# Kernel optimization log

Measured on AMD Instinct MI355X. Metric: run time of the kernel, lower is better.

## Reference

```python
import jax, jax.numpy as jnp
import numpy as np

B, IN_NUM, IN_DIM = 64, 4096, 8
NUM_CAPS, DIM_CAPS, ROUTINGS = 32, 16, 3
EPS = 1e-7  # keras.backend.epsilon()


def squash(v, axis=-1):
    # squash(s) = ||s||^2/(1+||s||^2) * s/||s||
    s2 = jnp.sum(v * v, axis=axis, keepdims=True)
    return (s2 / (1.0 + s2)) * v / jnp.sqrt(s2 + EPS)


def setup_inputs() -> dict:
    key = jax.random.key(0)
    k1, k2 = jax.random.split(key)
    inputs = jax.random.normal(k1, (B, IN_NUM, IN_DIM), dtype=jnp.float32)
    # kernel: [num_capsule, input_num_capsule, dim_capsule, input_dim_capsule]
    W = jax.random.normal(k2, (NUM_CAPS, IN_NUM, DIM_CAPS, IN_DIM), dtype=jnp.float32) * 0.05
    return {"inputs": inputs, "W": W}


def reference(inputs, W):
    # prediction vectors u_hat[b,c,n,j] = sum_i W[c,n,j,i] * x[b,n,i]
    hat = jnp.einsum('bni,cnji->bcnj', inputs, W)  # [B, C, N, D]
    b = jnp.zeros(hat.shape[:3], hat.dtype)        # routing logits [B, C, N]
    out = None
    for i in range(ROUTINGS):
        c = jax.nn.softmax(b, axis=1)              # couple over output capsules
        out = squash(jnp.einsum('bcn,bcnj->bcj', c, hat))  # [B, C, D]
        if i < ROUTINGS - 1:
            b = b + jnp.einsum('bcj,bcnj->bcn', out, hat)  # agreement update
    return out
```

## Files before the change

### kernel.cpp

```cpp
#include <hip/hip_runtime.h>
#include <math.h>


typedef __fp16 h2 __attribute__((ext_vector_type(2)));
typedef __fp16 half4 __attribute__((ext_vector_type(4)));
typedef float f32x16 __attribute__((ext_vector_type(16)));

union U2 { h2 h; unsigned u; };

__device__ __forceinline__ float fdot2(h2 a, h2 b, float c) {
    return __builtin_amdgcn_fdot2(a, b, c, false);
}
__device__ __forceinline__ h2 uash2(unsigned u) { U2 t; t.u = u; return t.h; }


template <int NPB>
__global__ __launch_bounds__(512, 4) void pass0_kernel(
    const float* __restrict__ W,
    const float* __restrict__ x,
    ushort* __restrict__ Wh,
    ushort* __restrict__ xh,
    unsigned* __restrict__ partial)
{
    constexpr int NB = 4096 / NPB;
    const int bid = blockIdx.x;
    const int half = bid / NB, nblk = bid % NB;
    const int n0 = nblk * NPB;
    const int t = threadIdx.x, l = t & 63, w = t >> 6;
    const int bl = l & 31, hi = l >> 5;
    const int cj = half * 256 + w * 32 + bl;

    __shared__ __align__(16) ushort xs[NPB * 512];
    __shared__ unsigned sep[8192];

    #pragma unroll
    for (int rep = 0; rep < NPB / 4; ++rep) {
        const int idx = t + rep * 512;
        const int b = idx / (2 * NPB), f4 = idx % (2 * NPB);
        const int nl = f4 >> 1, isl = f4 & 1;
        float4 v = *reinterpret_cast<const float4*>(
            x + (size_t)b * 32768 + (size_t)n0 * 8 + f4 * 4);
        half4 h;
        h[0] = (__fp16)v.x; h[1] = (__fp16)v.y; h[2] = (__fp16)v.z; h[3] = (__fp16)v.w;
        const int slot = (nl * 128 + b * 2 + isl) ^ ((nl & 7) << 1) ^ ((b >> 3) & 3);
        *reinterpret_cast<half4*>(xs + slot * 4) = h;
    }
    __syncthreads();

    if (half == 0) {
        #pragma unroll
        for (int rep = 0; rep < NPB / 4; ++rep) {
            const int u = t + rep * 512;
            const int nl = u >> 7, b = (u >> 1) & 63, isl = u & 1;
            const int slot = (nl * 128 + b * 2 + isl) ^ ((nl & 7) << 1) ^ ((b >> 3) & 3);
            half4 h = *reinterpret_cast<const half4*>(xs + slot * 4);
            *reinterpret_cast<half4*>(xh + (size_t)n0 * 512 + u * 4) = h;
        }
    }

    const float* wb = W + (size_t)(cj >> 4) * 524288 + (size_t)n0 * 128 + (cj & 15) * 8 + hi * 4;
    ushort* whp = Wh + ((size_t)n0 * 512 + cj) * 8 + hi * 4;

    f32x16 acc0 = {}, acc1 = {};
    float4 wv = *reinterpret_cast<const float4*>(wb);
    #pragma unroll 1
    for (int s = 0; s < NPB; ++s) {
        float4 wvn;
        if (s < NPB - 1)
            wvn = *reinterpret_cast<const float4*>(wb + (s + 1) * 128);
        const int sw = ((s & 7) << 1) ^ ((bl >> 3) & 3);
        const int slot0 = (s * 128 + bl * 2 + hi) ^ sw;
        const int slot1 = (s * 128 + bl * 2 + 64 + hi) ^ sw;
        half4 b0 = *reinterpret_cast<const half4*>(xs + slot0 * 4);
        half4 b1 = *reinterpret_cast<const half4*>(xs + slot1 * 4);
        half4 a;
        a[0] = (__fp16)wv.x; a[1] = (__fp16)wv.y; a[2] = (__fp16)wv.z; a[3] = (__fp16)wv.w;
        *reinterpret_cast<half4*>(whp + (size_t)s * 4096) = a;
        acc0 = __builtin_amdgcn_mfma_f32_32x32x8f16(a, b0, acc0, 0, 0, 0);
        acc1 = __builtin_amdgcn_mfma_f32_32x32x8f16(a, b1, acc1, 0, 0, 0);
        wv = wvn;
    }
    #pragma unroll
    for (int r = 0; r < 16; ++r) { acc0[r] *= 0.03125f; acc1[r] *= 0.03125f; }

    #pragma unroll
    for (int hb = 0; hb < 2; ++hb) {
        #pragma unroll
        for (int q = 0; q < 8; ++q) {
            const float e0 = hb ? acc1[2 * q] : acc0[2 * q];
            const float e1 = hb ? acc1[2 * q + 1] : acc0[2 * q + 1];
            U2 u; u.h = __builtin_amdgcn_cvt_pkrtz(e0, e1);
            const int cjp = w * 16 + 4 * (q >> 1) + (q & 1) + 2 * hi;
            const int bb = bl + 32 * hb;
            sep[bb * 128 + (cjp ^ bb)] = u.u;
        }
    }
    __syncthreads();
    #pragma unroll
    for (int u2 = 0; u2 < 16; ++u2) {
        const int idx = t + u2 * 512;
        const int ub = idx >> 7, ucjp = idx & 127;
        partial[(size_t)((ub >> 5) * NB + nblk) * 8192 + (ub & 31) * 256 + half * 128 + ucjp]
            = sep[ub * 128 + (ucjp ^ ub)];
    }
}


template <int NPB>
__global__ __launch_bounds__(512, 4) void pass12_kernel(
    const ushort* __restrict__ Wh,
    const ushort* __restrict__ xh,
    const ushort* __restrict__ OcumG,
    unsigned* __restrict__ partial)
{
    constexpr int NB = 4096 / NPB;
    const int bid = blockIdx.x;
    const int bt = bid / NB, nblk = bid % NB;
    const int n0 = nblk * NPB;
    const int t = threadIdx.x, l = t & 63, w = t >> 6;
    const int bl = l & 31, hi = l >> 5;
    const int b = bt * 32 + bl;

    __shared__ __align__(16) float pd[2][2][32][12];
    __shared__ unsigned sep[8192];

    const int cj0 = w * 64 + bl, cj1 = cj0 + 32;
    const ushort* xb = xh + ((size_t)n0 * 64 + b) * 8 + hi * 4;
    const ushort* whp0 = Wh + ((size_t)n0 * 512 + cj0) * 8 + hi * 4;
    const ushort* whp1 = Wh + ((size_t)n0 * 512 + cj1) * 8 + hi * 4;

    h2 oc[2][8];
    {
        const unsigned* og = reinterpret_cast<const unsigned*>(OcumG);
        #pragma unroll
        for (int mt = 0; mt < 2; ++mt) {
            const int cA = 4 * w + 2 * mt;
            const unsigned idx = (unsigned)b * 256 + cA * 8 + hi * 2;
            oc[mt][0] = uash2(og[idx]);      oc[mt][1] = uash2(og[idx + 1]);
            oc[mt][2] = uash2(og[idx + 4]);  oc[mt][3] = uash2(og[idx + 5]);
            oc[mt][4] = uash2(og[idx + 8]);  oc[mt][5] = uash2(og[idx + 9]);
            oc[mt][6] = uash2(og[idx + 12]); oc[mt][7] = uash2(og[idx + 13]);
        }
    }

    f32x16 zero = {};
    h2 acc0h[8], acc1h[8];
    #pragma unroll
    for (int q = 0; q < 8; ++q) {
        acc0h[q] = (h2)(__fp16)0.f;
        acc1h[q] = (h2)(__fp16)0.f;
    }

    half4 a0A = *reinterpret_cast<const half4*>(whp0);
    half4 a1A = *reinterpret_cast<const half4*>(whp1);
    half4 bfA = *reinterpret_cast<const half4*>(xb);
    half4 a0B = *reinterpret_cast<const half4*>(whp0 + 4096);
    half4 a1B = *reinterpret_cast<const half4*>(whp1 + 4096);
    half4 bfB = *reinterpret_cast<const half4*>(xb + 512);

    #pragma unroll 1
    for (int p = 0; p < NPB / 2; ++p) {
        half4 a0An, a1An, bfAn, a0Bn, a1Bn, bfBn;
        if (p < NPB / 2 - 1) {
            const int sA = 2 * p + 2, sB = 2 * p + 3;
            a0An = *reinterpret_cast<const half4*>(whp0 + (size_t)sA * 4096);
            a1An = *reinterpret_cast<const half4*>(whp1 + (size_t)sA * 4096);
            bfAn = *reinterpret_cast<const half4*>(xb + (size_t)sA * 512);
            a0Bn = *reinterpret_cast<const half4*>(whp0 + (size_t)sB * 4096);
            a1Bn = *reinterpret_cast<const half4*>(whp1 + (size_t)sB * 4096);
            bfBn = *reinterpret_cast<const half4*>(xb + (size_t)sB * 512);
        }
        h2 hA0[8], hA1[8];
        {
            f32x16 d0 = __builtin_amdgcn_mfma_f32_32x32x8f16(a0A, bfA, zero, 0, 0, 0);
            f32x16 d1 = __builtin_amdgcn_mfma_f32_32x32x8f16(a1A, bfA, zero, 0, 0, 0);
            #pragma unroll
            for (int q = 0; q < 8; ++q) {
                hA0[q] = __builtin_amdgcn_cvt_pkrtz(d0[2 * q], d0[2 * q + 1]);
                hA1[q] = __builtin_amdgcn_cvt_pkrtz(d1[2 * q], d1[2 * q + 1]);
            }
        }
        float pA0_A = fdot2(hA0[3], oc[0][3], fdot2(hA0[2], oc[0][2], fdot2(hA0[1], oc[0][1], fdot2(hA0[0], oc[0][0], 0.f))));
        float pB0_A = fdot2(hA0[7], oc[0][7], fdot2(hA0[6], oc[0][6], fdot2(hA0[5], oc[0][5], fdot2(hA0[4], oc[0][4], 0.f))));
        float pA1_A = fdot2(hA1[3], oc[1][3], fdot2(hA1[2], oc[1][2], fdot2(hA1[1], oc[1][1], fdot2(hA1[0], oc[1][0], 0.f))));
        float pB1_A = fdot2(hA1[7], oc[1][7], fdot2(hA1[6], oc[1][6], fdot2(hA1[5], oc[1][5], fdot2(hA1[4], oc[1][4], 0.f))));
        h2 hB0[8], hB1[8];
        {
            f32x16 d0 = __builtin_amdgcn_mfma_f32_32x32x8f16(a0B, bfB, zero, 0, 0, 0);
            f32x16 d1 = __builtin_amdgcn_mfma_f32_32x32x8f16(a1B, bfB, zero, 0, 0, 0);
            #pragma unroll
            for (int q = 0; q < 8; ++q) {
                hB0[q] = __builtin_amdgcn_cvt_pkrtz(d0[2 * q], d0[2 * q + 1]);
                hB1[q] = __builtin_amdgcn_cvt_pkrtz(d1[2 * q], d1[2 * q + 1]);
            }
        }
        float pA0_B = fdot2(hB0[3], oc[0][3], fdot2(hB0[2], oc[0][2], fdot2(hB0[1], oc[0][1], fdot2(hB0[0], oc[0][0], 0.f))));
        float pB0_B = fdot2(hB0[7], oc[0][7], fdot2(hB0[6], oc[0][6], fdot2(hB0[5], oc[0][5], fdot2(hB0[4], oc[0][4], 0.f))));
        float pA1_B = fdot2(hB1[3], oc[1][3], fdot2(hB1[2], oc[1][2], fdot2(hB1[1], oc[1][1], fdot2(hB1[0], oc[1][0], 0.f))));
        float pB1_B = fdot2(hB1[7], oc[1][7], fdot2(hB1[6], oc[1][6], fdot2(hB1[5], oc[1][5], fdot2(hB1[4], oc[1][4], 0.f))));

        pA0_A += __shfl_xor(pA0_A, 32, 64);
        pB0_A += __shfl_xor(pB0_A, 32, 64);
        pA1_A += __shfl_xor(pA1_A, 32, 64);
        pB1_A += __shfl_xor(pB1_A, 32, 64);
        pA0_B += __shfl_xor(pA0_B, 32, 64);
        pB0_B += __shfl_xor(pB0_B, 32, 64);
        pA1_B += __shfl_xor(pA1_B, 32, 64);
        pB1_B += __shfl_xor(pB1_B, 32, 64);

        float eA0_A = __expf(pA0_A), eB0_A = __expf(pB0_A);
        float eA1_A = __expf(pA1_A), eB1_A = __expf(pB1_A);
        float eA0_B = __expf(pA0_B), eB0_B = __expf(pB0_B);
        float eA1_B = __expf(pA1_B), eB1_B = __expf(pB1_B);

        const int buf = p & 1;
        if (l < 32) {
            pd[buf][0][bl][w] = eA0_A + eB0_A + eA1_A + eB1_A;
            pd[buf][1][bl][w] = eA0_B + eB0_B + eA1_B + eB1_B;
        }
        __syncthreads();
        const float4 qa0 = *reinterpret_cast<const float4*>(&pd[buf][0][bl][0]);
        const float4 qa1 = *reinterpret_cast<const float4*>(&pd[buf][0][bl][4]);
        const float4 qb0 = *reinterpret_cast<const float4*>(&pd[buf][1][bl][0]);
        const float4 qb1 = *reinterpret_cast<const float4*>(&pd[buf][1][bl][4]);
        const float rdA = __builtin_amdgcn_rcpf(qa0.x + qa0.y + qa0.z + qa0.w +
                                                qa1.x + qa1.y + qa1.z + qa1.w);
        const float rdB = __builtin_amdgcn_rcpf(qb0.x + qb0.y + qb0.z + qb0.w +
                                                qb1.x + qb1.y + qb1.z + qb1.w);

        h2 c0A, c1A, c0B, c1B, c2A, c3A, c2B, c3B;
        c0A.x = (__fp16)(eA0_A * rdA); c0A.y = c0A.x;
        c1A.x = (__fp16)(eB0_A * rdA); c1A.y = c1A.x;
        c2A.x = (__fp16)(eA1_A * rdA); c2A.y = c2A.x;
        c3A.x = (__fp16)(eB1_A * rdA); c3A.y = c3A.x;
        c0B.x = (__fp16)(eA0_B * rdB); c0B.y = c0B.x;
        c1B.x = (__fp16)(eB0_B * rdB); c1B.y = c1B.x;
        c2B.x = (__fp16)(eA1_B * rdB); c2B.y = c2B.x;
        c3B.x = (__fp16)(eB1_B * rdB); c3B.y = c3B.x;

        #pragma unroll
        for (int q = 0; q < 4; ++q) {
            acc0h[q] = hA0[q] * c0A + acc0h[q];
            acc0h[q + 4] = hA0[q + 4] * c1A + acc0h[q + 4];
            acc1h[q] = hA1[q] * c2A + acc1h[q];
            acc1h[q + 4] = hA1[q + 4] * c3A + acc1h[q + 4];
        }
        #pragma unroll
        for (int q = 0; q < 4; ++q) {
            acc0h[q] = hB0[q] * c0B + acc0h[q];
            acc0h[q + 4] = hB0[q + 4] * c1B + acc0h[q + 4];
            acc1h[q] = hB1[q] * c2B + acc1h[q];
            acc1h[q + 4] = hB1[q + 4] * c3B + acc1h[q + 4];
        }
        a0A = a0An; a1A = a1An; bfA = bfAn;
        a0B = a0Bn; a1B = a1Bn; bfB = bfBn;
    }

    __syncthreads();
    #pragma unroll
    for (int mt = 0; mt < 2; ++mt) {
        #pragma unroll
        for (int q = 0; q < 8; ++q) {
            U2 u; u.h = mt ? acc1h[q] : acc0h[q];
            const int cjp = w * 32 + mt * 16 + 4 * (q >> 1) + (q & 1) + 2 * hi;
            sep[bl * 256 + (cjp ^ bl)] = u.u;
        }
    }
    __syncthreads();
    const unsigned gbase = (unsigned)bid * 8192;
    #pragma unroll
    for (int u2 = 0; u2 < 16; ++u2) {
        const int idx = t + u2 * 512;
        const int ubl = idx >> 8, ucjp = idx & 255;
        partial[gbase + idx] = sep[ubl * 256 + (ucjp ^ ubl)];
    }
}


template <int NB>
__global__ __launch_bounds__(256) void reduce_squash(const unsigned* __restrict__ partial32,
                                                     ushort* __restrict__ OcumG,
                                                     float* __restrict__ out,
                                                     int passIdx) {
    const int gtid = blockIdx.x * 256 + threadIdx.x;
    const int oid = gtid >> 2, sub = gtid & 3;
    const int b = oid >> 8, cjp = oid & 255;
    const int bt = b >> 5, bl = b & 31;
    const unsigned base = (unsigned)bt * (unsigned)NB * 8192u + (unsigned)bl * 256u + (unsigned)cjp;
    float sx = 0.f, sy = 0.f;
    #pragma unroll 8
    for (int i = 0; i < NB / 4; ++i) {
        U2 v; v.u = partial32[base + (unsigned)(sub + 4 * i) * 8192u];
        sx += (float)v.h.x;
        sy += (float)v.h.y;
    }
    sx += __shfl_xor(sx, 1, 64); sy += __shfl_xor(sy, 1, 64);
    sx += __shfl_xor(sx, 2, 64); sy += __shfl_xor(sy, 2, 64);
    float s2 = sx * sx + sy * sy;
    s2 += __shfl_xor(s2, 4, 64);
    s2 += __shfl_xor(s2, 8, 64);
    s2 += __shfl_xor(s2, 16, 64);
    float scale = (s2 / (1.f + s2)) / sqrtf(s2 + 1e-7f);
    float o0 = scale * sx, o1 = scale * sy;

    if (sub == 0) {
        unsigned* ocp = reinterpret_cast<unsigned*>(OcumG) + b * 256 + cjp;
        float a0 = o0, a1 = o1;
        if (passIdx) {
            U2 old; old.u = *ocp;
            a0 += (float)old.h.x;
            a1 += (float)old.h.y;
        }
        U2 nw; nw.h = __builtin_amdgcn_cvt_pkrtz(a0, a1);
        *ocp = nw.u;
        if (passIdx == 2) {
            out[b * 512 + cjp * 2] = o0;
            out[b * 512 + cjp * 2 + 1] = o1;
        }
    }
}


extern "C" void kernel_launch(void* const* d_in, const int* in_sizes, int n_in,
                              void* d_out, int out_size, void* d_ws, size_t ws_size,
                              hipStream_t stream) {
    const float* x = (const float*)d_in[0];
    const float* W = (const float*)d_in[1];
    float* out = (float*)d_out;

    char* ws = (char*)d_ws;
    ushort* Wh = (ushort*)ws;
    const size_t MiB = 1024 * 1024;

    if (ws_size >= 52 * MiB + 65536) {
        unsigned* partialU = (unsigned*)(ws + 32 * MiB);
        ushort* xh = (ushort*)(ws + 48 * MiB);
        ushort* OcumG = (ushort*)(ws + 52 * MiB);
        pass0_kernel<16><<<512, 512, 0, stream>>>(W, x, Wh, xh, partialU);
        reduce_squash<256><<<256, 256, 0, stream>>>(partialU, OcumG, out, 0);
        pass12_kernel<16><<<512, 512, 0, stream>>>(Wh, xh, OcumG, partialU);
        reduce_squash<256><<<256, 256, 0, stream>>>(partialU, OcumG, out, 1);
        pass12_kernel<16><<<512, 512, 0, stream>>>(Wh, xh, OcumG, partialU);
        reduce_squash<256><<<256, 256, 0, stream>>>(partialU, OcumG, out, 2);
    } else {
        unsigned* partialU = (unsigned*)(ws + 32 * MiB);
        ushort* xh = (ushort*)(ws + 40 * MiB);
        ushort* OcumG = (ushort*)(ws + 44 * MiB);
        pass0_kernel<32><<<256, 512, 0, stream>>>(W, x, Wh, xh, partialU);
        reduce_squash<128><<<256, 256, 0, stream>>>(partialU, OcumG, out, 0);
        pass12_kernel<32><<<256, 512, 0, stream>>>(Wh, xh, OcumG, partialU);
        reduce_squash<128><<<256, 256, 0, stream>>>(partialU, OcumG, out, 1);
        pass12_kernel<32><<<256, 512, 0, stream>>>(Wh, xh, OcumG, partialU);
        reduce_squash<128><<<256, 256, 0, stream>>>(partialU, OcumG, out, 2);
    }
}
```

Before: 167.6 us.

## Fuse reduce-squash into pass kernels via last-blocks atomic ticket

After: 516.1 us. +207.9%, slower.

```diff
diff --git a/kernel.cpp b/kernel.cpp
--- a/kernel.cpp
+++ b/kernel.cpp
@@ -13,276 +13,12 @@
 }
 __device__ __forceinline__ h2 uash2(unsigned u) { U2 t; t.u = u; return t.h; }
 
-
-template <int NPB>
-__global__ __launch_bounds__(512, 4) void pass0_kernel(
-    const float* __restrict__ W,
-    const float* __restrict__ x,
-    ushort* __restrict__ Wh,
-    ushort* __restrict__ xh,
-    unsigned* __restrict__ partial)
-{
-    constexpr int NB = 4096 / NPB;
-    const int bid = blockIdx.x;
-    const int half = bid / NB, nblk = bid % NB;
-    const int n0 = nblk * NPB;
-    const int t = threadIdx.x, l = t & 63, w = t >> 6;
-    const int bl = l & 31, hi = l >> 5;
-    const int cj = half * 256 + w * 32 + bl;
-
-    __shared__ __align__(16) ushort xs[NPB * 512];
-    __shared__ unsigned sep[8192];
-
-    #pragma unroll
-    for (int rep = 0; rep < NPB / 4; ++rep) {
-        const int idx = t + rep * 512;
-        const int b = idx / (2 * NPB), f4 = idx % (2 * NPB);
-        const int nl = f4 >> 1, isl = f4 & 1;
-        float4 v = *reinterpret_cast<const float4*>(
-            x + (size_t)b * 32768 + (size_t)n0 * 8 + f4 * 4);
-        half4 h;
-        h[0] = (__fp16)v.x; h[1] = (__fp16)v.y; h[2] = (__fp16)v.z; h[3] = (__fp16)v.w;
-        const int slot = (nl * 128 + b * 2 + isl) ^ ((nl & 7) << 1) ^ ((b >> 3) & 3);
-        *reinterpret_cast<half4*>(xs + slot * 4) = h;
-    }
-    __syncthreads();
-
-    if (half == 0) {
-        #pragma unroll
-        for (int rep = 0; rep < NPB / 4; ++rep) {
-            const int u = t + rep * 512;
-            const int nl = u >> 7, b = (u >> 1) & 63, isl = u & 1;
-            const int slot = (nl * 128 + b * 2 + isl) ^ ((nl & 7) << 1) ^ ((b >> 3) & 3);
-            half4 h = *reinterpret_cast<const half4*>(xs + slot * 4);
-            *reinterpret_cast<half4*>(xh + (size_t)n0 * 512 + u * 4) = h;
-        }
-    }
-
-    const float* wb = W + (size_t)(cj >> 4) * 524288 + (size_t)n0 * 128 + (cj & 15) * 8 + hi * 4;
-    ushort* whp = Wh + ((size_t)n0 * 512 + cj) * 8 + hi * 4;
-
-    f32x16 acc0 = {}, acc1 = {};
-    float4 wv = *reinterpret_cast<const float4*>(wb);
-    #pragma unroll 1
-    for (int s = 0; s < NPB; ++s) {
-        float4 wvn;
-        if (s < NPB - 1)
-            wvn = *reinterpret_cast<const float4*>(wb + (s + 1) * 128);
-        const int sw = ((s & 7) << 1) ^ ((bl >> 3) & 3);
-        const int slot0 = (s * 128 + bl * 2 + hi) ^ sw;
-        const int slot1 = (s * 128 + bl * 2 + 64 + hi) ^ sw;
-        half4 b0 = *reinterpret_cast<const half4*>(xs + slot0 * 4);
-        half4 b1 = *reinterpret_cast<const half4*>(xs + slot1 * 4);
-        half4 a;
-        a[0] = (__fp16)wv.x; a[1] = (__fp16)wv.y; a[2] = (__fp16)wv.z; a[3] = (__fp16)wv.w;
-        *reinterpret_cast<half4*>(whp + (size_t)s * 4096) = a;
-        acc0 = __builtin_amdgcn_mfma_f32_32x32x8f16(a, b0, acc0, 0, 0, 0);
-        acc1 = __builtin_amdgcn_mfma_f32_32x32x8f16(a, b1, acc1, 0, 0, 0);
-        wv = wvn;
-    }
-    #pragma unroll
-    for (int r = 0; r < 16; ++r) { acc0[r] *= 0.03125f; acc1[r] *= 0.03125f; }
-
-    #pragma unroll
-    for (int hb = 0; hb < 2; ++hb) {
-        #pragma unroll
-        for (int q = 0; q < 8; ++q) {
-            const float e0 = hb ? acc1[2 * q] : acc0[2 * q];
-            const float e1 = hb ? acc1[2 * q + 1] : acc0[2 * q + 1];
-            U2 u; u.h = __builtin_amdgcn_cvt_pkrtz(e0, e1);
-            const int cjp = w * 16 + 4 * (q >> 1) + (q & 1) + 2 * hi;
-            const int bb = bl + 32 * hb;
-            sep[bb * 128 + (cjp ^ bb)] = u.u;
-        }
-    }
-    __syncthreads();
-    #pragma unroll
-    for (int u2 = 0; u2 < 16; ++u2) {
-        const int idx = t + u2 * 512;
-        const int ub = idx >> 7, ucjp = idx & 127;
-        partial[(size_t)((ub >> 5) * NB + nblk) * 8192 + (ub & 31) * 256 + half * 128 + ucjp]
-            = sep[ub * 128 + (ucjp ^ ub)];
-    }
-}
-
-
-template <int NPB>
-__global__ __launch_bounds__(512, 4) void pass12_kernel(
-    const ushort* __restrict__ Wh,
-    const ushort* __restrict__ xh,
-    const ushort* __restrict__ OcumG,
-    unsigned* __restrict__ partial)
-{
-    constexpr int NB = 4096 / NPB;
-    const int bid = blockIdx.x;
-    const int bt = bid / NB, nblk = bid % NB;
-    const int n0 = nblk * NPB;
-    const int t = threadIdx.x, l = t & 63, w = t >> 6;
-    const int bl = l & 31, hi = l >> 5;
-    const int b = bt * 32 + bl;
-
-    __shared__ __align__(16) float pd[2][2][32][12];
-    __shared__ unsigned sep[8192];
-
-    const int cj0 = w * 64 + bl, cj1 = cj0 + 32;
-    const ushort* xb = xh + ((size_t)n0 * 64 + b) * 8 + hi * 4;
-    const ushort* whp0 = Wh + ((size_t)n0 * 512 + cj0) * 8 + hi * 4;
-    const ushort* whp1 = Wh + ((size_t)n0 * 512 + cj1) * 8 + hi * 4;
-
-    h2 oc[2][8];
-    {
-        const unsigned* og = reinterpret_cast<const unsigned*>(OcumG);
-        #pragma unroll
-        for (int mt = 0; mt < 2; ++mt) {
-            const int cA = 4 * w + 2 * mt;
-            const unsigned idx = (unsigned)b * 256 + cA * 8 + hi * 2;
-            oc[mt][0] = uash2(og[idx]);      oc[mt][1] = uash2(og[idx + 1]);
-            oc[mt][2] = uash2(og[idx + 4]);  oc[mt][3] = uash2(og[idx + 5]);
-            oc[mt][4] = uash2(og[idx + 8]);  oc[mt][5] = uash2(og[idx + 9]);
-            oc[mt][6] = uash2(og[idx + 12]); oc[mt][7] = uash2(og[idx + 13]);
-        }
-    }
-
-    f32x16 zero = {};
-    h2 acc0h[8], acc1h[8];
-    #pragma unroll
-    for (int q = 0; q < 8; ++q) {
-        acc0h[q] = (h2)(__fp16)0.f;
-        acc1h[q] = (h2)(__fp16)0.f;
-    }
-
-    half4 a0A = *reinterpret_cast<const half4*>(whp0);
-    half4 a1A = *reinterpret_cast<const half4*>(whp1);
-    half4 bfA = *reinterpret_cast<const half4*>(xb);
-    half4 a0B = *reinterpret_cast<const half4*>(whp0 + 4096);
-    half4 a1B = *reinterpret_cast<const half4*>(whp1 + 4096);
-    half4 bfB = *reinterpret_cast<const half4*>(xb + 512);
-
-    #pragma unroll 1
-    for (int p = 0; p < NPB / 2; ++p) {
-        half4 a0An, a1An, bfAn, a0Bn, a1Bn, bfBn;
-        if (p < NPB / 2 - 1) {
-            const int sA = 2 * p + 2, sB = 2 * p + 3;
-            a0An = *reinterpret_cast<const half4*>(whp0 + (size_t)sA * 4096);
-            a1An = *reinterpret_cast<const half4*>(whp1 + (size_t)sA * 4096);
-            bfAn = *reinterpret_cast<const half4*>(xb + (size_t)sA * 512);
-            a0Bn = *reinterpret_cast<const half4*>(whp0 + (size_t)sB * 4096);
-            a1Bn = *reinterpret_cast<const half4*>(whp1 + (size_t)sB * 4096);
-            bfBn = *reinterpret_cast<const half4*>(xb + (size_t)sB * 512);
-        }
-        h2 hA0[8], hA1[8];
-        {
-            f32x16 d0 = __builtin_amdgcn_mfma_f32_32x32x8f16(a0A, bfA, zero, 0, 0, 0);
-            f32x16 d1 = __builtin_amdgcn_mfma_f32_32x32x8f16(a1A, bfA, zero, 0, 0, 0);
-            #pragma unroll
-            for (int q = 0; q < 8; ++q) {
-                hA0[q] = __builtin_amdgcn_cvt_pkrtz(d0[2 * q], d0[2 * q + 1]);
-                hA1[q] = __builtin_amdgcn_cvt_pkrtz(d1[2 * q], d1[2 * q + 1]);
-            }
-        }
-        float pA0_A = fdot2(hA0[3], oc[0][3], fdot2(hA0[2], oc[0][2], fdot2(hA0[1], oc[0][1], fdot2(hA0[0], oc[0][0], 0.f))));
-        float pB0_A = fdot2(hA0[7], oc[0][7], fdot2(hA0[6], oc[0][6], fdot2(hA0[5], oc[0][5], fdot2(hA0[4], oc[0][4], 0.f))));
-        float pA1_A = fdot2(hA1[3], oc[1][3], fdot2(hA1[2], oc[1][2], fdot2(hA1[1], oc[1][1], fdot2(hA1[0], oc[1][0], 0.f))));
-        float pB1_A = fdot2(hA1[7], oc[1][7], fdot2(hA1[6], oc[1][6], fdot2(hA1[5], oc[1][5], fdot2(hA1[4], oc[1][4], 0.f))));
-        h2 hB0[8], hB1[8];
-        {
-            f32x16 d0 = __builtin_amdgcn_mfma_f32_32x32x8f16(a0B, bfB, zero, 0, 0, 0);
-            f32x16 d1 = __builtin_amdgcn_mfma_f32_32x32x8f16(a1B, bfB, zero, 0, 0, 0);
-            #pragma unroll
-            for (int q = 0; q < 8; ++q) {
-                hB0[q] = __builtin_amdgcn_cvt_pkrtz(d0[2 * q], d0[2 * q + 1]);
-                hB1[q] = __builtin_amdgcn_cvt_pkrtz(d1[2 * q], d1[2 * q + 1]);
-            }
-        }
-        float pA0_B = fdot2(hB0[3], oc[0][3], fdot2(hB0[2], oc[0][2], fdot2(hB0[1], oc[0][1], fdot2(hB0[0], oc[0][0], 0.f))));
-        float pB0_B = fdot2(hB0[7], oc[0][7], fdot2(hB0[6], oc[0][6], fdot2(hB0[5], oc[0][5], fdot2(hB0[4], oc[0][4], 0.f))));
-        float pA1_B = fdot2(hB1[3], oc[1][3], fdot2(hB1[2], oc[1][2], fdot2(hB1[1], oc[1][1], fdot2(hB1[0], oc[1][0], 0.f))));
-        float pB1_B = fdot2(hB1[7], oc[1][7], fdot2(hB1[6], oc[1][6], fdot2(hB1[5], oc[1][5], fdot2(hB1[4], oc[1][4], 0.f))));
-
-        pA0_A += __shfl_xor(pA0_A, 32, 64);
-        pB0_A += __shfl_xor(pB0_A, 32, 64);
-        pA1_A += __shfl_xor(pA1_A, 32, 64);
-        pB1_A += __shfl_xor(pB1_A, 32, 64);
-        pA0_B += __shfl_xor(pA0_B, 32, 64);
-        pB0_B += __shfl_xor(pB0_B, 32, 64);
-        pA1_B += __shfl_xor(pA1_B, 32, 64);
-        pB1_B += __shfl_xor(pB1_B, 32, 64);
-
-        float eA0_A = __expf(pA0_A), eB0_A = __expf(pB0_A);
-        float eA1_A = __expf(pA1_A), eB1_A = __expf(pB1_A);
-        float eA0_B = __expf(pA0_B), eB0_B = __expf(pB0_B);
-        float eA1_B = __expf(pA1_B), eB1_B = __expf(pB1_B);
-
-        const int buf = p & 1;
-        if (l < 32) {
-            pd[buf][0][bl][w] = eA0_A + eB0_A + eA1_A + eB1_A;
-            pd[buf][1][bl][w] = eA0_B + eB0_B + eA1_B + eB1_B;
-        }
-        __syncthreads();
-        const float4 qa0 = *reinterpret_cast<const float4*>(&pd[buf][0][bl][0]);
-        const float4 qa1 = *reinterpret_cast<const float4*>(&pd[buf][0][bl][4]);
-        const float4 qb0 = *reinterpret_cast<const float4*>(&pd[buf][1][bl][0]);
-        const float4 qb1 = *reinterpret_cast<const float4*>(&pd[buf][1][bl][4]);
-        const float rdA = __builtin_amdgcn_rcpf(qa0.x + qa0.y + qa0.z + qa0.w +
-                                                qa1.x + qa1.y + qa1.z + qa1.w);
-        const float rdB = __builtin_amdgcn_rcpf(qb0.x + qb0.y + qb0.z + qb0.w +
-                                                qb1.x + qb1.y + qb1.z + qb1.w);
-
-        h2 c0A, c1A, c0B, c1B, c2A, c3A, c2B, c3B;
-        c0A.x = (__fp16)(eA0_A * rdA); c0A.y = c0A.x;
-        c1A.x = (__fp16)(eB0_A * rdA); c1A.y = c1A.x;
-        c2A.x = (__fp16)(eA1_A * rdA); c2A.y = c2A.x;
-        c3A.x = (__fp16)(eB1_A * rdA); c3A.y = c3A.x;
-        c0B.x = (__fp16)(eA0_B * rdB); c0B.y = c0B.x;
-        c1B.x = (__fp16)(eB0_B * rdB); c1B.y = c1B.x;
-        c2B.x = (__fp16)(eA1_B * rdB); c2B.y = c2B.x;
-        c3B.x = (__fp16)(eB1_B * rdB); c3B.y = c3B.x;
-
-        #pragma unroll
-        for (int q = 0; q < 4; ++q) {
-            acc0h[q] = hA0[q] * c0A + acc0h[q];
-            acc0h[q + 4] = hA0[q + 4] * c1A + acc0h[q + 4];
-            acc1h[q] = hA1[q] * c2A + acc1h[q];
-            acc1h[q + 4] = hA1[q + 4] * c3A + acc1h[q + 4];
-        }
-        #pragma unroll
-        for (int q = 0; q < 4; ++q) {
-            acc0h[q] = hB0[q] * c0B + acc0h[q];
-            acc0h[q + 4] = hB0[q + 4] * c1B + acc0h[q + 4];
-            acc1h[q] = hB1[q] * c2B + acc1h[q];
-            acc1h[q + 4] = hB1[q + 4] * c3B + acc1h[q + 4];
-        }
-        a0A = a0An; a1A = a1An; bfA = bfAn;
-        a0B = a0Bn; a1B = a1Bn; bfB = bfBn;
-    }
-
-    __syncthreads();
-    #pragma unroll
-    for (int mt = 0; mt < 2; ++mt) {
-        #pragma unroll
-        for (int q = 0; q < 8; ++q) {
-            U2 u; u.h = mt ? acc1h[q] : acc0h[q];
-            const int cjp = w * 32 + mt * 16 + 4 * (q >> 1) + (q & 1) + 2 * hi;
-            sep[bl * 256 + (cjp ^ bl)] = u.u;
-        }
-    }
-    __syncthreads();
-    const unsigned gbase = (unsigned)bid * 8192;
-    #pragma unroll
-    for (int u2 = 0; u2 < 16; ++u2) {
-        const int idx = t + u2 * 512;
-        const int ubl = idx >> 8, ucjp = idx & 255;
-        partial[gbase + idx] = sep[ubl * 256 + (ucjp ^ ubl)];
-    }
-}
-
-
 template <int NB>
-__global__ __launch_bounds__(256) void reduce_squash(const unsigned* __restrict__ partial32,
-                                                     ushort* __restrict__ OcumG,
-                                                     float* __restrict__ out,
-                                                     int passIdx) {
-    const int gtid = blockIdx.x * 256 + threadIdx.x;
+__device__ __forceinline__ void reduce_body(const unsigned* __restrict__ partial32,
+                                            ushort* __restrict__ OcumG,
+                                            float* __restrict__ out,
+                                            int passIdx, int slice, int t) {
+    const int gtid = slice * 512 + t;
     const int oid = gtid >> 2, sub = gtid & 3;
     const int b = oid >> 8, cjp = oid & 255;
     const int bt = b >> 5, bl = b & 31;
@@ -321,6 +57,282 @@
 }
 
 
+template <int PASS, int NPB>
+__global__ __launch_bounds__(512, 4) void fused(
+    const float* __restrict__ W,
+    const float* __restrict__ x,
+    ushort* __restrict__ Wh,
+    ushort* __restrict__ xh,
+    ushort* __restrict__ OcumG,
+    unsigned* __restrict__ partial,
+    float* __restrict__ out,
+    unsigned* __restrict__ ctr)
+{
+    constexpr int NB = 4096 / NPB;
+    constexpr int NBLOCKS = 2 * NB;
+    const int bid = blockIdx.x;
+    const int t = threadIdx.x, l = t & 63, w = t >> 6;
+    const int bl = l & 31, hi = l >> 5;
+
+    __shared__ unsigned sep[8192];
+    __shared__ unsigned s_ticket;
+
+    if constexpr (PASS == 0) {
+        const int half = bid / NB, nblk = bid % NB;
+        const int n0 = nblk * NPB;
+        const int cj = half * 256 + w * 32 + bl;
+
+        __shared__ __align__(16) ushort xs[NPB * 512];
+
+        #pragma unroll
+        for (int rep = 0; rep < NPB / 4; ++rep) {
+            const int idx = t + rep * 512;
+            const int b = idx / (2 * NPB), f4 = idx % (2 * NPB);
+            const int nl = f4 >> 1, isl = f4 & 1;
+            float4 v = *reinterpret_cast<const float4*>(
+                x + (size_t)b * 32768 + (size_t)n0 * 8 + f4 * 4);
+            half4 h;
+            h[0] = (__fp16)v.x; h[1] = (__fp16)v.y; h[2] = (__fp16)v.z; h[3] = (__fp16)v.w;
+            const int slot = (nl * 128 + b * 2 + isl) ^ ((nl & 7) << 1) ^ ((b >> 3) & 3);
+            *reinterpret_cast<half4*>(xs + slot * 4) = h;
+        }
+        __syncthreads();
+
+        if (half == 0) {
+            #pragma unroll
+            for (int rep = 0; rep < NPB / 4; ++rep) {
+                const int u = t + rep * 512;
+                const int nl = u >> 7, b = (u >> 1) & 63, isl = u & 1;
+                const int slot = (nl * 128 + b * 2 + isl) ^ ((nl & 7) << 1) ^ ((b >> 3) & 3);
+                half4 h = *reinterpret_cast<const half4*>(xs + slot * 4);
+                *reinterpret_cast<half4*>(xh + (size_t)n0 * 512 + u * 4) = h;
+            }
+        }
+
+        const float* wb = W + (size_t)(cj >> 4) * 524288 + (size_t)n0 * 128 + (cj & 15) * 8 + hi * 4;
+        ushort* whp = Wh + ((size_t)n0 * 512 + cj) * 8 + hi * 4;
+
+        f32x16 acc0 = {}, acc1 = {};
+        float4 wv = *reinterpret_cast<const float4*>(wb);
+        #pragma unroll 1
+        for (int s = 0; s < NPB; ++s) {
+            float4 wvn;
+            if (s < NPB - 1)
+                wvn = *reinterpret_cast<const float4*>(wb + (s + 1) * 128);
+            const int sw = ((s & 7) << 1) ^ ((bl >> 3) & 3);
+            const int slot0 = (s * 128 + bl * 2 + hi) ^ sw;
+            const int slot1 = (s * 128 + bl * 2 + 64 + hi) ^ sw;
+            half4 b0 = *reinterpret_cast<const half4*>(xs + slot0 * 4);
+            half4 b1 = *reinterpret_cast<const half4*>(xs + slot1 * 4);
+            half4 a;
+            a[0] = (__fp16)wv.x; a[1] = (__fp16)wv.y; a[2] = (__fp16)wv.z; a[3] = (__fp16)wv.w;
+            *reinterpret_cast<half4*>(whp + (size_t)s * 4096) = a;
+            acc0 = __builtin_amdgcn_mfma_f32_32x32x8f16(a, b0, acc0, 0, 0, 0);
+            acc1 = __builtin_amdgcn_mfma_f32_32x32x8f16(a, b1, acc1, 0, 0, 0);
+            wv = wvn;
+        }
+        #pragma unroll
+        for (int r = 0; r < 16; ++r) { acc0[r] *= 0.03125f; acc1[r] *= 0.03125f; }
+
+        #pragma unroll
+        for (int hb = 0; hb < 2; ++hb) {
+            #pragma unroll
+            for (int q = 0; q < 8; ++q) {
+                const float e0 = hb ? acc1[2 * q] : acc0[2 * q];
+                const float e1 = hb ? acc1[2 * q + 1] : acc0[2 * q + 1];
+                U2 u; u.h = __builtin_amdgcn_cvt_pkrtz(e0, e1);
+                const int cjp = w * 16 + 4 * (q >> 1) + (q & 1) + 2 * hi;
+                const int bb = bl + 32 * hb;
+                sep[bb * 128 + (cjp ^ bb)] = u.u;
+            }
+        }
+        __syncthreads();
+        #pragma unroll
+        for (int u2 = 0; u2 < 16; ++u2) {
+            const int idx = t + u2 * 512;
+            const int ub = idx >> 7, ucjp = idx & 127;
+            partial[(size_t)((ub >> 5) * NB + nblk) * 8192 + (ub & 31) * 256 + half * 128 + ucjp]
+                = sep[ub * 128 + (ucjp ^ ub)];
+        }
+    } else {
+        const int bt = bid / NB, nblk = bid % NB;
+        const int n0 = nblk * NPB;
+        const int b = bt * 32 + bl;
+
+        __shared__ __align__(16) float pd[2][2][32][12];
+
+        const int cj0 = w * 64 + bl, cj1 = cj0 + 32;
+        const ushort* xb = xh + ((size_t)n0 * 64 + b) * 8 + hi * 4;
+        const ushort* whp0 = Wh + ((size_t)n0 * 512 + cj0) * 8 + hi * 4;
+        const ushort* whp1 = Wh + ((size_t)n0 * 512 + cj1) * 8 + hi * 4;
+
+        h2 oc[2][8];
+        {
+            const unsigned* og = reinterpret_cast<const unsigned*>(OcumG);
+            #pragma unroll
+            for (int mt = 0; mt < 2; ++mt) {
+                const int cA = 4 * w + 2 * mt;
+                const unsigned idx = (unsigned)b * 256 + cA * 8 + hi * 2;
+                oc[mt][0] = uash2(og[idx]);      oc[mt][1] = uash2(og[idx + 1]);
+                oc[mt][2] = uash2(og[idx + 4]);  oc[mt][3] = uash2(og[idx + 5]);
+                oc[mt][4] = uash2(og[idx + 8]);  oc[mt][5] = uash2(og[idx + 9]);
+                oc[mt][6] = uash2(og[idx + 12]); oc[mt][7] = uash2(og[idx + 13]);
+            }
+        }
+
+        f32x16 zero = {};
+        h2 acc0h[8], acc1h[8];
+        #pragma unroll
+        for (int q = 0; q < 8; ++q) {
+            acc0h[q] = (h2)(__fp16)0.f;
+            acc1h[q] = (h2)(__fp16)0.f;
+        }
+
+        half4 a0A = *reinterpret_cast<const half4*>(whp0);
+        half4 a1A = *reinterpret_cast<const half4*>(whp1);
+        half4 bfA = *reinterpret_cast<const half4*>(xb);
+        half4 a0B = *reinterpret_cast<const half4*>(whp0 + 4096);
+        half4 a1B = *reinterpret_cast<const half4*>(whp1 + 4096);
+        half4 bfB = *reinterpret_cast<const half4*>(xb + 512);
+
+        #pragma unroll 1
+        for (int p = 0; p < NPB / 2; ++p) {
+            half4 a0An, a1An, bfAn, a0Bn, a1Bn, bfBn;
+            if (p < NPB / 2 - 1) {
+                const int sA = 2 * p + 2, sB = 2 * p + 3;
+                a0An = *reinterpret_cast<const half4*>(whp0 + (size_t)sA * 4096);
+                a1An = *reinterpret_cast<const half4*>(whp1 + (size_t)sA * 4096);
+                bfAn = *reinterpret_cast<const half4*>(xb + (size_t)sA * 512);
+                a0Bn = *reinterpret_cast<const half4*>(whp0 + (size_t)sB * 4096);
+                a1Bn = *reinterpret_cast<const half4*>(whp1 + (size_t)sB * 4096);
+                bfBn = *reinterpret_cast<const half4*>(xb + (size_t)sB * 512);
+            }
+            h2 hA0[8], hA1[8];
+            {
+                f32x16 d0 = __builtin_amdgcn_mfma_f32_32x32x8f16(a0A, bfA, zero, 0, 0, 0);
+                f32x16 d1 = __builtin_amdgcn_mfma_f32_32x32x8f16(a1A, bfA, zero, 0, 0, 0);
+                #pragma unroll
+                for (int q = 0; q < 8; ++q) {
+                    hA0[q] = __builtin_amdgcn_cvt_pkrtz(d0[2 * q], d0[2 * q + 1]);
+                    hA1[q] = __builtin_amdgcn_cvt_pkrtz(d1[2 * q], d1[2 * q + 1]);
+                }
+            }
+            float pA0_A = fdot2(hA0[3], oc[0][3], fdot2(hA0[2], oc[0][2], fdot2(hA0[1], oc[0][1], fdot2(hA0[0], oc[0][0], 0.f))));
+            float pB0_A = fdot2(hA0[7], oc[0][7], fdot2(hA0[6], oc[0][6], fdot2(hA0[5], oc[0][5], fdot2(hA0[4], oc[0][4], 0.f))));
+            float pA1_A = fdot2(hA1[3], oc[1][3], fdot2(hA1[2], oc[1][2], fdot2(hA1[1], oc[1][1], fdot2(hA1[0], oc[1][0], 0.f))));
+            float pB1_A = fdot2(hA1[7], oc[1][7], fdot2(hA1[6], oc[1][6], fdot2(hA1[5], oc[1][5], fdot2(hA1[4], oc[1][4], 0.f))));
+            h2 hB0[8], hB1[8];
+            {
+                f32x16 d0 = __builtin_amdgcn_mfma_f32_32x32x8f16(a0B, bfB, zero, 0, 0, 0);
+                f32x16 d1 = __builtin_amdgcn_mfma_f32_32x32x8f16(a1B, bfB, zero, 0, 0, 0);
+                #pragma unroll
+                for (int q = 0; q < 8; ++q) {
+                    hB0[q] = __builtin_amdgcn_cvt_pkrtz(d0[2 * q], d0[2 * q + 1]);
+                    hB1[q] = __builtin_amdgcn_cvt_pkrtz(d1[2 * q], d1[2 * q + 1]);
+                }
+            }
+            float pA0_B = fdot2(hB0[3], oc[0][3], fdot2(hB0[2], oc[0][2], fdot2(hB0[1], oc[0][1], fdot2(hB0[0], oc[0][0], 0.f))));
+            float pB0_B = fdot2(hB0[7], oc[0][7], fdot2(hB0[6], oc[0][6], fdot2(hB0[5], oc[0][5], fdot2(hB0[4], oc[0][4], 0.f))));
+            float pA1_B = fdot2(hB1[3], oc[1][3], fdot2(hB1[2], oc[1][2], fdot2(hB1[1], oc[1][1], fdot2(hB1[0], oc[1][0], 0.f))));
+            float pB1_B = fdot2(hB1[7], oc[1][7], fdot2(hB1[6], oc[1][6], fdot2(hB1[5], oc[1][5], fdot2(hB1[4], oc[1][4], 0.f))));
+
+            pA0_A += __shfl_xor(pA0_A, 32, 64);
+            pB0_A += __shfl_xor(pB0_A, 32, 64);
+            pA1_A += __shfl_xor(pA1_A, 32, 64);
+            pB1_A += __shfl_xor(pB1_A, 32, 64);
+            pA0_B += __shfl_xor(pA0_B, 32, 64);
+            pB0_B += __shfl_xor(pB0_B, 32, 64);
+            pA1_B += __shfl_xor(pA1_B, 32, 64);
+            pB1_B += __shfl_xor(pB1_B, 32, 64);
+
+            float eA0_A = __expf(pA0_A), eB0_A = __expf(pB0_A);
+            float eA1_A = __expf(pA1_A), eB1_A = __expf(pB1_A);
+            float eA0_B = __expf(pA0_B), eB0_B = __expf(pB0_B);
+            float eA1_B = __expf(pA1_B), eB1_B = __expf(pB1_B);
+
+            const int buf = p & 1;
+            if (l < 32) {
+                pd[buf][0][bl][w] = eA0_A + eB0_A + eA1_A + eB1_A;
+                pd[buf][1][bl][w] = eA0_B + eB0_B + eA1_B + eB1_B;
+            }
+            __syncthreads();
+            const float4 qa0 = *reinterpret_cast<const float4*>(&pd[buf][0][bl][0]);
+            const float4 qa1 = *reinterpret_cast<const float4*>(&pd[buf][0][bl][4]);
+            const float4 qb0 = *reinterpret_cast<const float4*>(&pd[buf][1][bl][0]);
+            const float4 qb1 = *reinterpret_cast<const float4*>(&pd[buf][1][bl][4]);
+            const float rdA = __builtin_amdgcn_rcpf(qa0.x + qa0.y + qa0.z + qa0.w +
+                                                    qa1.x + qa1.y + qa1.z + qa1.w);
+            const float rdB = __builtin_amdgcn_rcpf(qb0.x + qb0.y + qb0.z + qb0.w +
+                                                    qb1.x + qb1.y + qb1.z + qb1.w);
+
+            h2 c0A, c1A, c0B, c1B, c2A, c3A, c2B, c3B;
+            c0A.x = (__fp16)(eA0_A * rdA); c0A.y = c0A.x;
+            c1A.x = (__fp16)(eB0_A * rdA); c1A.y = c1A.x;
+            c2A.x = (__fp16)(eA1_A * rdA); c2A.y = c2A.x;
+            c3A.x = (__fp16)(eB1_A * rdA); c3A.y = c3A.x;
+            c0B.x = (__fp16)(eA0_B * rdB); c0B.y = c0B.x;
+            c1B.x = (__fp16)(eB0_B * rdB); c1B.y = c1B.x;
+            c2B.x = (__fp16)(eA1_B * rdB); c2B.y = c2B.x;
+            c3B.x = (__fp16)(eB1_B * rdB); c3B.y = c3B.x;
+
+            #pragma unroll
+            for (int q = 0; q < 4; ++q) {
+                acc0h[q] = hA0[q] * c0A + acc0h[q];
+                acc0h[q + 4] = hA0[q + 4] * c1A + acc0h[q + 4];
+                acc1h[q] = hA1[q] * c2A + acc1h[q];
+                acc1h[q + 4] = hA1[q + 4] * c3A + acc1h[q + 4];
+            }
+            #pragma unroll
+            for (int q = 0; q < 4; ++q) {
+                acc0h[q] = hB0[q] * c0B + acc0h[q];
+                acc0h[q + 4] = hB0[q + 4] * c1B + acc0h[q + 4];
+                acc1h[q] = hB1[q] * c2B + acc1h[q];
+                acc1h[q + 4] = hB1[q + 4] * c3B + acc1h[q + 4];
+            }
+            a0A = a0An; a1A = a1An; bfA = bfAn;
+            a0B = a0Bn; a1B = a1Bn; bfB = bfBn;
+        }
+
+        __syncthreads();
+        #pragma unroll
+        for (int mt = 0; mt < 2; ++mt) {
+            #pragma unroll
+            for (int q = 0; q < 8; ++q) {
+                U2 u; u.h = mt ? acc1h[q] : acc0h[q];
+                const int cjp = w * 32 + mt * 16 + 4 * (q >> 1) + (q & 1) + 2 * hi;
+                sep[bl * 256 + (cjp ^ bl)] = u.u;
+            }
+        }
+        __syncthreads();
+        const unsigned gbase = (unsigned)bid * 8192;
+        #pragma unroll
+        for (int u2 = 0; u2 < 16; ++u2) {
+            const int idx = t + u2 * 512;
+            const int ubl = idx >> 8, ucjp = idx & 255;
+            partial[gbase + idx] = sep[ubl * 256 + (ucjp ^ ubl)];
+        }
+    }
+
+    __threadfence();
+    __syncthreads();
+    if (t == 0)
+        s_ticket = __hip_atomic_fetch_add(ctr, 1u, __ATOMIC_ACQ_REL,
+                                          __HIP_MEMORY_SCOPE_AGENT);
+    __syncthreads();
+    const unsigned ticket = s_ticket;
+    if (ticket >= (unsigned)(NBLOCKS - 128)) {
+        if (t == 0) {
+            while (__hip_atomic_load(ctr, __ATOMIC_ACQUIRE,
+                                     __HIP_MEMORY_SCOPE_AGENT) < (unsigned)NBLOCKS)
+                __builtin_amdgcn_s_sleep(2);
+        }
+        __syncthreads();
+        reduce_body<NB>(partial, OcumG, out, PASS,
+                        (int)(ticket - (unsigned)(NBLOCKS - 128)), t);
+    }
+}
+
+
 extern "C" void kernel_launch(void* const* d_in, const int* in_sizes, int n_in,
                               void* d_out, int out_size, void* d_ws, size_t ws_size,
                               hipStream_t stream) {
@@ -332,25 +344,23 @@
     ushort* Wh = (ushort*)ws;
     const size_t MiB = 1024 * 1024;
 
-    if (ws_size >= 52 * MiB + 65536) {
+    if (ws_size >= 52 * MiB + 65536 + 16) {
         unsigned* partialU = (unsigned*)(ws + 32 * MiB);
         ushort* xh = (ushort*)(ws + 48 * MiB);
         ushort* OcumG = (ushort*)(ws + 52 * MiB);
-        pass0_kernel<16><<<512, 512, 0, stream>>>(W, x, Wh, xh, partialU);
-        reduce_squash<256><<<256, 256, 0, stream>>>(partialU, OcumG, out, 0);
-        pass12_kernel<16><<<512, 512, 0, stream>>>(Wh, xh, OcumG, partialU);
-        reduce_squash<256><<<256, 256, 0, stream>>>(partialU, OcumG, out, 1);
-        pass12_kernel<16><<<512, 512, 0, stream>>>(Wh, xh, OcumG, partialU);
-        reduce_squash<256><<<256, 256, 0, stream>>>(partialU, OcumG, out, 2);
+        unsigned* ctrs = (unsigned*)(ws + 52 * MiB + 65536);
+        hipMemsetAsync(ctrs, 0, 16, stream);
+        fused<0, 16><<<512, 512, 0, stream>>>(W, x, Wh, xh, OcumG, partialU, out, ctrs + 0);
+        fused<1, 16><<<512, 512, 0, stream>>>(W, x, Wh, xh, OcumG, partialU, out, ctrs + 1);
+        fused<2, 16><<<512, 512, 0, stream>>>(W, x, Wh, xh, OcumG, partialU, out, ctrs + 2);
     } else {
         unsigned* partialU = (unsigned*)(ws + 32 * MiB);
         ushort* xh = (ushort*)(ws + 40 * MiB);
         ushort* OcumG = (ushort*)(ws + 44 * MiB);
-        pass0_kernel<32><<<256, 512, 0, stream>>>(W, x, Wh, xh, partialU);
-        reduce_squash<128><<<256, 256, 0, stream>>>(partialU, OcumG, out, 0);
-        pass12_kernel<32><<<256, 512, 0, stream>>>(Wh, xh, OcumG, partialU);
-        reduce_squash<128><<<256, 256, 0, stream>>>(partialU, OcumG, out, 1);
-        pass12_kernel<32><<<256, 512, 0, stream>>>(Wh, xh, OcumG, partialU);
-        reduce_squash<128><<<256, 256, 0, stream>>>(partialU, OcumG, out, 2);
+        unsigned* ctrs = (unsigned*)(ws + 44 * MiB + 65536);
+        hipMemsetAsync(ctrs, 0, 16, stream);
+        fused<0, 32><<<256, 512, 0, stream>>>(W, x, Wh, xh, OcumG, partialU, out, ctrs + 0);
+        fused<1, 32><<<256, 512, 0, stream>>>(W, x, Wh, xh, OcumG, partialU, out, ctrs + 1);
+        fused<2, 32><<<256, 512, 0, stream>>>(W, x, Wh, xh, OcumG, partialU, out, ctrs + 2);
     }
 }
```

## Alias shared buffers, raise occupancy, and split N into smaller blocks

Applied to the files above, without the earlier changes.

After: 350.7 us. 109% more time.

```diff
diff --git a/kernel.cpp b/kernel.cpp
--- a/kernel.cpp
+++ b/kernel.cpp
@@ -15,7 +15,7 @@
 
 
 template <int NPB>
-__global__ __launch_bounds__(512, 4) void pass0_kernel(
+__global__ __launch_bounds__(512, 8) void pass0_kernel(
     const float* __restrict__ W,
     const float* __restrict__ x,
     ushort* __restrict__ Wh,
@@ -30,8 +30,9 @@
     const int bl = l & 31, hi = l >> 5;
     const int cj = half * 256 + w * 32 + bl;
 
-    __shared__ __align__(16) ushort xs[NPB * 512];
-    __shared__ unsigned sep[8192];
+    __shared__ __align__(16) unsigned shbuf[8192];
+    ushort* xs = reinterpret_cast<ushort*>(shbuf);
+    unsigned* sep = shbuf;
 
     #pragma unroll
     for (int rep = 0; rep < NPB / 4; ++rep) {
@@ -83,6 +84,7 @@
     #pragma unroll
     for (int r = 0; r < 16; ++r) { acc0[r] *= 0.03125f; acc1[r] *= 0.03125f; }
 
+    __syncthreads();
     #pragma unroll
     for (int hb = 0; hb < 2; ++hb) {
         #pragma unroll
@@ -107,7 +109,7 @@
 
 
 template <int NPB>
-__global__ __launch_bounds__(512, 4) void pass12_kernel(
+__global__ __launch_bounds__(512, 8) void pass12_kernel(
     const ushort* __restrict__ Wh,
     const ushort* __restrict__ xh,
     const ushort* __restrict__ OcumG,
@@ -121,8 +123,9 @@
     const int bl = l & 31, hi = l >> 5;
     const int b = bt * 32 + bl;
 
-    __shared__ __align__(16) float pd[2][2][32][12];
-    __shared__ unsigned sep[8192];
+    __shared__ __align__(16) unsigned shbuf[8192];
+    float* pd = reinterpret_cast<float*>(shbuf);
+    unsigned* sep = shbuf;
 
     const int cj0 = w * 64 + bl, cj1 = cj0 + 32;
     const ushort* xb = xh + ((size_t)n0 * 64 + b) * 8 + hi * 4;
@@ -215,14 +218,14 @@
 
         const int buf = p & 1;
         if (l < 32) {
-            pd[buf][0][bl][w] = eA0_A + eB0_A + eA1_A + eB1_A;
-            pd[buf][1][bl][w] = eA0_B + eB0_B + eA1_B + eB1_B;
+            pd[((buf * 2 + 0) * 32 + bl) * 12 + w] = eA0_A + eB0_A + eA1_A + eB1_A;
+            pd[((buf * 2 + 1) * 32 + bl) * 12 + w] = eA0_B + eB0_B + eA1_B + eB1_B;
         }
         __syncthreads();
-        const float4 qa0 = *reinterpret_cast<const float4*>(&pd[buf][0][bl][0]);
-        const float4 qa1 = *reinterpret_cast<const float4*>(&pd[buf][0][bl][4]);
-        const float4 qb0 = *reinterpret_cast<const float4*>(&pd[buf][1][bl][0]);
-        const float4 qb1 = *reinterpret_cast<const float4*>(&pd[buf][1][bl][4]);
+        const float4 qa0 = *reinterpret_cast<const float4*>(&pd[((buf * 2 + 0) * 32 + bl) * 12 + 0]);
+        const float4 qa1 = *reinterpret_cast<const float4*>(&pd[((buf * 2 + 0) * 32 + bl) * 12 + 4]);
+        const float4 qb0 = *reinterpret_cast<const float4*>(&pd[((buf * 2 + 1) * 32 + bl) * 12 + 0]);
+        const float4 qb1 = *reinterpret_cast<const float4*>(&pd[((buf * 2 + 1) * 32 + bl) * 12 + 4]);
         const float rdA = __builtin_amdgcn_rcpf(qa0.x + qa0.y + qa0.z + qa0.w +
                                                 qa1.x + qa1.y + qa1.z + qa1.w);
         const float rdB = __builtin_amdgcn_rcpf(qb0.x + qb0.y + qb0.z + qb0.w +
@@ -277,29 +280,30 @@
 }
 
 
-template <int NB>
+template <int NB, int SUB>
 __global__ __launch_bounds__(256) void reduce_squash(const unsigned* __restrict__ partial32,
                                                      ushort* __restrict__ OcumG,
                                                      float* __restrict__ out,
                                                      int passIdx) {
     const int gtid = blockIdx.x * 256 + threadIdx.x;
-    const int oid = gtid >> 2, sub = gtid & 3;
+    const int oid = gtid / SUB, sub = gtid % SUB;
     const int b = oid >> 8, cjp = oid & 255;
     const int bt = b >> 5, bl = b & 31;
     const unsigned base = (unsigned)bt * (unsigned)NB * 8192u + (unsigned)bl * 256u + (unsigned)cjp;
     float sx = 0.f, sy = 0.f;
     #pragma unroll 8
-    for (int i = 0; i < NB / 4; ++i) {
-        U2 v; v.u = partial32[base + (unsigned)(sub + 4 * i) * 8192u];
+    for (int i = 0; i < NB / SUB; ++i) {
+        U2 v; v.u = partial32[base + (unsigned)(sub + SUB * i) * 8192u];
         sx += (float)v.h.x;
         sy += (float)v.h.y;
     }
     sx += __shfl_xor(sx, 1, 64); sy += __shfl_xor(sy, 1, 64);
     sx += __shfl_xor(sx, 2, 64); sy += __shfl_xor(sy, 2, 64);
+    if constexpr (SUB == 8) { sx += __shfl_xor(sx, 4, 64); sy += __shfl_xor(sy, 4, 64); }
     float s2 = sx * sx + sy * sy;
-    s2 += __shfl_xor(s2, 4, 64);
-    s2 += __shfl_xor(s2, 8, 64);
-    s2 += __shfl_xor(s2, 16, 64);
+    s2 += __shfl_xor(s2, SUB, 64);
+    s2 += __shfl_xor(s2, 2 * SUB, 64);
+    s2 += __shfl_xor(s2, 4 * SUB, 64);
     float scale = (s2 / (1.f + s2)) / sqrtf(s2 + 1e-7f);
     float o0 = scale * sx, o1 = scale * sy;
 
@@ -332,25 +336,25 @@
     ushort* Wh = (ushort*)ws;
     const size_t MiB = 1024 * 1024;
 
-    if (ws_size >= 52 * MiB + 65536) {
+    if (ws_size >= 68 * MiB + 65536) {
+        unsigned* partialU = (unsigned*)(ws + 32 * MiB);
+        ushort* xh = (ushort*)(ws + 64 * MiB);
+        ushort* OcumG = (ushort*)(ws + 68 * MiB);
+        pass0_kernel<8><<<1024, 512, 0, stream>>>(W, x, Wh, xh, partialU);
+        reduce_squash<512, 8><<<512, 256, 0, stream>>>(partialU, OcumG, out, 0);
+        pass12_kernel<8><<<1024, 512, 0, stream>>>(Wh, xh, OcumG, partialU);
+        reduce_squash<512, 8><<<512, 256, 0, stream>>>(partialU, OcumG, out, 1);
+        pass12_kernel<8><<<1024, 512, 0, stream>>>(Wh, xh, OcumG, partialU);
+        reduce_squash<512, 8><<<512, 256, 0, stream>>>(partialU, OcumG, out, 2);
+    } else {
         unsigned* partialU = (unsigned*)(ws + 32 * MiB);
         ushort* xh = (ushort*)(ws + 48 * MiB);
         ushort* OcumG = (ushort*)(ws + 52 * MiB);
         pass0_kernel<16><<<512, 512, 0, stream>>>(W, x, Wh, xh, partialU);
-        reduce_squash<256><<<256, 256, 0, stream>>>(partialU, OcumG, out, 0);
+        reduce_squash<256, 4><<<256, 256, 0, stream>>>(partialU, OcumG, out, 0);
         pass12_kernel<16><<<512, 512, 0, stream>>>(Wh, xh, OcumG, partialU);
-        reduce_squash<256><<<256, 256, 0, stream>>>(partialU, OcumG, out, 1);
+        reduce_squash<256, 4><<<256, 256, 0, stream>>>(partialU, OcumG, out, 1);
         pass12_kernel<16><<<512, 512, 0, stream>>>(Wh, xh, OcumG, partialU);
-        reduce_squash<256><<<256, 256, 0, stream>>>(partialU, OcumG, out, 2);
-    } else {
-        unsigned* partialU = (unsigned*)(ws + 32 * MiB);
-        ushort* xh = (ushort*)(ws + 40 * MiB);
-        ushort* OcumG = (ushort*)(ws + 44 * MiB);
-        pass0_kernel<32><<<256, 512, 0, stream>>>(W, x, Wh, xh, partialU);
-        reduce_squash<128><<<256, 256, 0, stream>>>(partialU, OcumG, out, 0);
-        pass12_kernel<32><<<256, 512, 0, stream>>>(Wh, xh, OcumG, partialU);
-        reduce_squash<128><<<256, 256, 0, stream>>>(partialU, OcumG, out, 1);
-        pass12_kernel<32><<<256, 512, 0, stream>>>(Wh, xh, OcumG, partialU);
-        reduce_squash<128><<<256, 256, 0, stream>>>(partialU, OcumG, out, 2);
-    }
-}
+        reduce_squash<256, 4><<<256, 256, 0, stream>>>(partialU, OcumG, out, 2);
+    }
+}
```
